# Optimization experiments

Measured on AMD Instinct MI355X. Metric: run time of the kernel, lower is better.

## Reference

```python
import jax, jax.numpy as jnp
import numpy as np

HIDDEN = 4096
NUM_Q = 32
NUM_KV = 8
HEAD_DIM = 128
EPS = 1e-6
ROPE_THETA = 1e6


def _rmsnorm(x, w):
    # x: [..., HEAD_DIM]
    var = jnp.mean(x * x, axis=-1, keepdims=True)
    return x * jax.lax.rsqrt(var + EPS) * w


def _rope(x, positions):
    # x: [n_tok, H, HEAD_DIM], rotate-half convention
    half = HEAD_DIM // 2
    inv_freq = 1.0 / (ROPE_THETA ** (jnp.arange(0, half, dtype=jnp.float32) / half))
    freqs = positions.astype(jnp.float32)[:, None] * inv_freq  # [n_tok, half]
    cos = jnp.concatenate([jnp.cos(freqs), jnp.cos(freqs)], axis=-1)[:, None, :]
    sin = jnp.concatenate([jnp.sin(freqs), jnp.sin(freqs)], axis=-1)[:, None, :]
    x1, x2 = x[..., :half], x[..., half:]
    rot = jnp.concatenate([-x2, x1], axis=-1)
    return x * cos + rot * sin


def setup_inputs() -> dict:
    key = jax.random.key(0)
    ks = jax.random.split(key, 7)
    n_tok = 2048
    s = 0.02
    return {
        "hidden": jax.random.normal(ks[0], (n_tok, HIDDEN), dtype=jnp.float32),
        "positions": jnp.arange(n_tok, dtype=jnp.int32),
        "Wq": jax.random.normal(ks[1], (HIDDEN, NUM_Q * HEAD_DIM), dtype=jnp.float32) * s,
        "Wk": jax.random.normal(ks[2], (HIDDEN, NUM_KV * HEAD_DIM), dtype=jnp.float32) * s,
        "Wv": jax.random.normal(ks[3], (HIDDEN, NUM_KV * HEAD_DIM), dtype=jnp.float32) * s,
        "Wo": jax.random.normal(ks[4], (NUM_Q * HEAD_DIM, HIDDEN), dtype=jnp.float32) * s,
        "q_norm_w": jnp.ones((HEAD_DIM,), dtype=jnp.float32),
        "k_norm_w": jnp.ones((HEAD_DIM,), dtype=jnp.float32),
    }


def reference(hidden, positions, Wq, Wk, Wv, Wo, q_norm_w, k_norm_w):
    n_tok = hidden.shape[0]
    group = NUM_Q // NUM_KV

    q = (hidden @ Wq).reshape(n_tok, NUM_Q, HEAD_DIM)
    k = (hidden @ Wk).reshape(n_tok, NUM_KV, HEAD_DIM)
    v = (hidden @ Wv).reshape(n_tok, NUM_KV, HEAD_DIM)

    q = _rmsnorm(q, q_norm_w)
    k = _rmsnorm(k, k_norm_w)
    q = _rope(q, positions)
    k = _rope(k, positions)

    # GQA: group q heads [n_tok, NUM_KV, group, HEAD_DIM]
    qg = q.reshape(n_tok, NUM_KV, group, HEAD_DIM)
    scale = 1.0 / np.sqrt(HEAD_DIM)
    scores = jnp.einsum("qhgd,khd->hgqk", qg, k) * scale  # [NUM_KV, group, n_tok, n_tok]
    causal = jnp.tril(jnp.ones((n_tok, n_tok), dtype=bool))
    scores = jnp.where(causal, scores, jnp.finfo(scores.dtype).min)
    probs = jax.nn.softmax(scores, axis=-1)
    out = jnp.einsum("hgqk,khd->qhgd", probs, v)  # [n_tok, NUM_KV, group, HEAD_DIM]
    out = out.reshape(n_tok, NUM_Q * HEAD_DIM)
    return out @ Wo
```

## Files before the change

kernel.cpp:

```cpp
#include <hip/hip_runtime.h>
#include <stdint.h>

typedef unsigned short u16;
typedef __bf16 bf16_t;
typedef bf16_t bf16x8 __attribute__((ext_vector_type(8)));
typedef float f32x4 __attribute__((ext_vector_type(4)));
typedef float f32x16 __attribute__((ext_vector_type(16)));
typedef u16 u16x4 __attribute__((ext_vector_type(4)));
typedef u16 u16x8 __attribute__((ext_vector_type(8)));
typedef uint32_t u32x4 __attribute__((ext_vector_type(4)));
typedef int i32x2 __attribute__((ext_vector_type(2)));

#define HIDDEN 4096
#define NTOK 2048
#define NQ 32
#define NKV 8
#define HD 128
#define QKV_N 6144

#define AS1 __attribute__((address_space(1)))
#define AS3 __attribute__((address_space(3)))

__device__ __forceinline__ u16 f2bf(float f) {
  union { float f; uint32_t u; } v; v.f = f;
  uint32_t u = v.u;
  return (u16)((u + 0x7fffu + ((u >> 16) & 1u)) >> 16);
}

__global__ void cvt_hidden(const float* __restrict__ src, u16* __restrict__ dst, int n4) {
  int i = blockIdx.x * blockDim.x + threadIdx.x;
  if (i >= n4) return;
  float4 v = ((const float4*)src)[i];
  u16x4 o;
  o[0] = f2bf(v.x); o[1] = f2bf(v.y); o[2] = f2bf(v.z); o[3] = f2bf(v.w);
  ((u16x4*)dst)[i] = o;
}

__global__ void transpose_cvt(const float* __restrict__ src, u16* __restrict__ dst,
                              int R, int C) {
  __shared__ float tile[64][65];
  int tx = threadIdx.x & 63;
  int ty = threadIdx.x >> 6;
  int r0 = blockIdx.y * 64, c0 = blockIdx.x * 64;
  for (int i = 0; i < 16; i++) {
    int r = ty + i * 4;
    tile[r][tx] = src[(size_t)(r0 + r) * C + c0 + tx];
  }
  __syncthreads();
  for (int i = 0; i < 16; i++) {
    int c = ty + i * 4;
    dst[(size_t)(c0 + c) * R + r0 + tx] = f2bf(tile[tx][c]);
  }
}

__global__ __launch_bounds__(256, 3) void gemm_bt(const u16* __restrict__ A,
                                                  const u16* __restrict__ B,
                                                  float* __restrict__ C,
                                                  int M, int N, int K) {
  __shared__ u16 sA[128 * 64];
  __shared__ u16 sB[128 * 64];
  const int tid = threadIdx.x;
  const int wave = tid >> 6, lane = tid & 63;
  const int quad = lane >> 4, l16 = lane & 15;
  const int wy = wave >> 1, wx = wave & 1;
  const int row0 = blockIdx.y * 128, col0 = blockIdx.x * 128;
  f32x4 acc[4][4] = {};
  const int lr = lane >> 3;
  const int sc = (lane & 7) ^ lr;
  const u16* gA = A + (size_t)(row0 + wave * 32 + lr) * K + sc * 8;
  const u16* gB = B + (size_t)(col0 + wave * 32 + lr) * K + sc * 8;
  u16* lA = sA + wave * 32 * 64;
  u16* lB = sB + wave * 32 * 64;
  const int swz = l16 & 7;
  for (int k0 = 0; k0 < K; k0 += 64) {
    for (int j = 0; j < 4; j++) {
      __builtin_amdgcn_global_load_lds(
          (AS1 void*)(void*)(gA + k0 + (size_t)(j * 8) * K),
          (AS3 void*)(void*)(lA + j * 8 * 64), 16, 0, 0);
      __builtin_amdgcn_global_load_lds(
          (AS1 void*)(void*)(gB + k0 + (size_t)(j * 8) * K),
          (AS3 void*)(void*)(lB + j * 8 * 64), 16, 0, 0);
    }
    __syncthreads();
    bf16x8 af[2][4], bfr[2][4];
    for (int s = 0; s < 2; s++)
      for (int mi = 0; mi < 4; mi++) {
        const int c = ((s * 4 + quad) ^ swz) * 8;
        af[s][mi] = *(const bf16x8*)(const void*)(sA + (wy * 64 + mi * 16 + l16) * 64 + c);
        bfr[s][mi] = *(const bf16x8*)(const void*)(sB + (wx * 64 + mi * 16 + l16) * 64 + c);
      }
    for (int s = 0; s < 2; s++)
      for (int mi = 0; mi < 4; mi++)
        for (int ni = 0; ni < 4; ni++)
          acc[mi][ni] = __builtin_amdgcn_mfma_f32_16x16x32_bf16(af[s][mi], bfr[s][ni], acc[mi][ni], 0, 0, 0);
    __syncthreads();
  }
  for (int mi = 0; mi < 4; mi++)
    for (int ni = 0; ni < 4; ni++) {
      int row = row0 + wy * 64 + mi * 16 + quad * 4;
      int col = col0 + wx * 64 + ni * 16 + l16;
      float* cp = C + (size_t)row * N + col;
      for (int r = 0; r < 4; r++) cp[(size_t)r * N] = acc[mi][ni][r];
    }
}

__global__ void normrope(const float* __restrict__ qkv, const int* __restrict__ pos,
                         const float* __restrict__ qw, const float* __restrict__ kw,
                         u16* __restrict__ Qo, u16* __restrict__ Ko) {
  const int hh = blockIdx.x;
  const int t = blockIdx.y * 4 + (threadIdx.x >> 6);
  const int lane = threadIdx.x & 63;
  const bool isQ = hh < NQ;
  const int col = isQ ? hh * HD : HIDDEN + (hh - NQ) * HD;
  const float* src = qkv + (size_t)t * QKV_N + col;
  float x1 = src[lane], x2 = src[lane + 64];
  float ss = x1 * x1 + x2 * x2;
  for (int m = 1; m < 64; m <<= 1) ss += __shfl_xor(ss, m);
  float inv = rsqrtf(ss * (1.0f / 128.0f) + 1e-6f);
  const float* w = isQ ? qw : kw;
  x1 *= inv * w[lane];
  x2 *= inv * w[lane + 64];
  float p = (float)pos[t];
  float freq = expf((float)lane * -0.2158673525f);
  float a = p * freq;
  float sn = sinf(a), cs = cosf(a);
  float o1 = x1 * cs - x2 * sn;
  float o2 = x2 * cs + x1 * sn;
  const float osc = isQ ? 0.08838834764831845f : 1.0f;
  u16* dst = isQ ? (Qo + (size_t)t * (NQ * HD) + hh * HD)
                 : (Ko + (size_t)t * (NKV * HD) + (hh - NQ) * HD);
  dst[lane] = f2bf(o1 * osc);
  dst[lane + 64] = f2bf(o2 * osc);
}

__global__ void vtrans(const float* __restrict__ qkv, u16* __restrict__ vT) {
  __shared__ float s[128][65];
  int tb = blockIdx.x;
  int vh = blockIdx.y;
  int tid = threadIdx.x;
  for (int i = 0; i < 32; i++) {
    int e = i * 256 + tid;
    int tl = e >> 7;
    int d = e & 127;
    s[d][tl] = qkv[(size_t)(tb * 64 + tl) * QKV_N + 5120 + vh * 128 + d];
  }
  __syncthreads();
  for (int i = 0; i < 32; i++) {
    int e = i * 256 + tid;
    int d = e >> 6;
    int tl = e & 63;
    vT[(size_t)vh * (HD * NTOK) + (size_t)d * NTOK + tb * 64 + tl] = f2bf(s[d][tl]);
  }
}

__global__ __launch_bounds__(512, 2) void flash3(const u16* __restrict__ Q,
                                                 const u16* __restrict__ K,
                                                 const u16* __restrict__ V,
                                                 u16* __restrict__ O) {
  __shared__ u16 sK[64 * 136];
  __shared__ u16 sV[128 * 72];
  const int lid = blockIdx.x;
  const int kvh = lid & 7;
  const int head = kvh * 4 + ((lid >> 3) & 3);
  const int p = lid >> 5;
  const int tid = threadIdx.x;
  const int wave = tid >> 6, lane = tid & 63;
  const int l32 = lane & 31, h = lane >> 5;
  const int tileq = (wave < 4) ? p : (15 - p);
  const int qrow0 = tileq * 128 + (wave & 3) * 32;
  const u16* Vh = V + (size_t)kvh * (HD * NTOK);

  bf16x8 qf[8];
  const u16* qbase = Q + (size_t)(qrow0 + l32) * (NQ * HD) + head * HD + h * 8;
#pragma unroll
  for (int ks = 0; ks < 8; ks++)
    qf[ks] = *(const bf16x8*)(const void*)(qbase + ks * 16);

  f32x16 accO[4] = {};
  float l_loc = 0.f;
  const int nU = 32 - 2 * p;
  const int rk0 = tid >> 4, ck0 = tid & 15;
  const int rv0 = tid >> 3, cv0 = tid & 7;
  const u16* Kr = K + (size_t)kvh * HD + ck0 * 8;
  const u16* Vr = Vh + (size_t)rv0 * NTOK + cv0 * 8;
  const u16* Vr2 = Vh + (size_t)(rv0 + 64) * NTOK + cv0 * 8;

  u16x8 k0 = *(const u16x8*)(const void*)(Kr + (size_t)rk0 * (NKV * HD));
  u16x8 k1 = *(const u16x8*)(const void*)(Kr + (size_t)(rk0 + 32) * (NKV * HD));
  u16x8 v0 = *(const u16x8*)(const void*)(Vr);
  u16x8 v1 = *(const u16x8*)(const void*)(Vr2);

  for (int kb = 0; kb < nU; kb++) {
    __syncthreads();
    *(u16x8*)(void*)(sK + rk0 * 136 + ck0 * 8) = k0;
    *(u16x8*)(void*)(sK + (rk0 + 32) * 136 + ck0 * 8) = k1;
    *(u16x8*)(void*)(sV + rv0 * 72 + cv0 * 8) = v0;
    *(u16x8*)(void*)(sV + (rv0 + 64) * 72 + cv0 * 8) = v1;
    __syncthreads();
    if (kb + 1 < nU) {
      const size_t koff = (size_t)((kb + 1) * 64) * (NKV * HD);
      k0 = *(const u16x8*)(const void*)(Kr + koff + (size_t)rk0 * (NKV * HD));
      k1 = *(const u16x8*)(const void*)(Kr + koff + (size_t)(rk0 + 32) * (NKV * HD));
      v0 = *(const u16x8*)(const void*)(Vr + (kb + 1) * 64);
      v1 = *(const u16x8*)(const void*)(Vr2 + (kb + 1) * 64);
    }
    const int t0 = kb * 64;
    if (t0 > qrow0 + 31) continue;
    const bool act1 = (t0 + 32 <= qrow0 + 31);

    f32x16 s0 = {}, s1 = {};
#pragma unroll
    for (int ks = 0; ks < 8; ks++) {
      bf16x8 kf0 = *(const bf16x8*)(const void*)(sK + l32 * 136 + ks * 16 + h * 8);
      s0 = __builtin_amdgcn_mfma_f32_32x32x16_bf16(kf0, qf[ks], s0, 0, 0, 0);
    }
    if (act1) {
#pragma unroll
      for (int ks = 0; ks < 8; ks++) {
        bf16x8 kf1 = *(const bf16x8*)(const void*)(sK + (32 + l32) * 136 + ks * 16 + h * 8);
        s1 = __builtin_amdgcn_mfma_f32_32x32x16_bf16(kf1, qf[ks], s1, 0, 0, 0);
      }
    }

    auto process = [&](const f32x16& sv_, int tb) {
      float pr[16];
      const int tbase = t0 + tb * 32;
      const int qg = qrow0 + l32;
      if (tbase + 31 <= qrow0) {
#pragma unroll
        for (int r = 0; r < 16; r++) { float e = __expf(sv_[r]); pr[r] = e; l_loc += e; }
      } else {
#pragma unroll
        for (int r = 0; r < 16; r++) {
          const int tok = tbase + (r & 3) + 8 * (r >> 2) + 4 * h;
          float e = (tok <= qg) ? __expf(sv_[r]) : 0.f;
          pr[r] = e; l_loc += e;
        }
      }
#pragma unroll
      for (int u = 0; u < 2; u++) {
        uint32_t A0, A1, B0, B1;
        asm("v_cvt_pk_bf16_f32 %0, %1, %2" : "=v"(A0) : "v"(pr[u * 8 + 0]), "v"(pr[u * 8 + 1]));
        asm("v_cvt_pk_bf16_f32 %0, %1, %2" : "=v"(A1) : "v"(pr[u * 8 + 2]), "v"(pr[u * 8 + 3]));
        asm("v_cvt_pk_bf16_f32 %0, %1, %2" : "=v"(B0) : "v"(pr[u * 8 + 4]), "v"(pr[u * 8 + 5]));
        asm("v_cvt_pk_bf16_f32 %0, %1, %2" : "=v"(B1) : "v"(pr[u * 8 + 6]), "v"(pr[u * 8 + 7]));
#if __has_builtin(__builtin_amdgcn_permlane32_swap)
        i32x2 r02 = __builtin_amdgcn_permlane32_swap((int)A0, (int)B0, false, false);
        i32x2 r13 = __builtin_amdgcn_permlane32_swap((int)A1, (int)B1, false, false);
        const uint32_t w0 = (uint32_t)r02.x, w2 = (uint32_t)r02.y;
        const uint32_t w1 = (uint32_t)r13.x, w3 = (uint32_t)r13.y;
#else
        const uint32_t A0x = (uint32_t)__shfl_xor((int)A0, 32);
        const uint32_t A1x = (uint32_t)__shfl_xor((int)A1, 32);
        const uint32_t B0x = (uint32_t)__shfl_xor((int)B0, 32);
        const uint32_t B1x = (uint32_t)__shfl_xor((int)B1, 32);
        const uint32_t w0 = h ? B0x : A0;
        const uint32_t w1 = h ? B1x : A1;
        const uint32_t w2 = h ? B0 : A0x;
        const uint32_t w3 = h ? B1 : A1x;
#endif
        union { u32x4 w; bf16x8 v; } pf;
        pf.w = (u32x4){w0, w1, w2, w3};
#pragma unroll
        for (int db = 0; db < 4; db++) {
          bf16x8 vf = *(const bf16x8*)(const void*)(sV + (db * 32 + l32) * 72 + tb * 32 + u * 16 + h * 8);
          accO[db] = __builtin_amdgcn_mfma_f32_32x32x16_bf16(vf, pf.v, accO[db], 0, 0, 0);
        }
      }
    };
    process(s0, 0);
    if (act1) process(s1, 1);
  }

  l_loc += __shfl_xor(l_loc, 32);
  const float inv = 1.0f / l_loc;
  u16* ob = O + (size_t)(qrow0 + l32) * (NQ * HD) + head * HD;
#pragma unroll
  for (int db = 0; db < 4; db++)
#pragma unroll
    for (int g = 0; g < 4; g++) {
      u16x4 o4;
#pragma unroll
      for (int j = 0; j < 4; j++) o4[j] = f2bf(accO[db][4 * g + j] * inv);
      *(u16x4*)(void*)(ob + db * 32 + g * 8 + h * 4) = o4;
    }
}

extern "C" void kernel_launch(void* const* d_in, const int* in_sizes, int n_in,
                              void* d_out, int out_size, void* d_ws, size_t ws_size,
                              hipStream_t stream) {
  const float* hidden = (const float*)d_in[0];
  const int* positions = (const int*)d_in[1];
  const float* Wq = (const float*)d_in[2];
  const float* Wk = (const float*)d_in[3];
  const float* Wv = (const float*)d_in[4];
  const float* Wo = (const float*)d_in[5];
  const float* qw = (const float*)d_in[6];
  const float* kw = (const float*)d_in[7];
  char* ws = (char*)d_ws;
  u16* hid_bf  = (u16*)(ws);
  u16* WqkvT   = (u16*)(ws + 16777216);
  u16* WoT     = (u16*)(ws + 67108864);
  float* qkvf  = (float*)(ws + 100663296);
  u16* Qn      = (u16*)(ws + 150994944);
  u16* Kn      = (u16*)(ws + 167772160);
  u16* Vt      = (u16*)(ws + 171966464);
  u16* AO      = (u16*)(ws + 176160768);
  float* outp  = (float*)d_out;

  cvt_hidden<<<NTOK * HIDDEN / 4 / 256, 256, 0, stream>>>(hidden, hid_bf, NTOK * HIDDEN / 4);
  transpose_cvt<<<dim3(64, 64), 256, 0, stream>>>(Wq, WqkvT, 4096, 4096);
  transpose_cvt<<<dim3(16, 64), 256, 0, stream>>>(Wk, WqkvT + (size_t)4096 * 4096, 4096, 1024);
  transpose_cvt<<<dim3(16, 64), 256, 0, stream>>>(Wv, WqkvT + (size_t)5120 * 4096, 4096, 1024);
  transpose_cvt<<<dim3(64, 64), 256, 0, stream>>>(Wo, WoT, 4096, 4096);
  gemm_bt<<<dim3(48, 16), 256, 0, stream>>>(hid_bf, WqkvT, qkvf, 2048, 6144, 4096);
  normrope<<<dim3(40, 512), 256, 0, stream>>>(qkvf, positions, qw, kw, Qn, Kn);
  vtrans<<<dim3(32, 8), 256, 0, stream>>>(qkvf, Vt);
  flash3<<<dim3(256), 512, 0, stream>>>(Qn, Kn, Vt, AO);
  gemm_bt<<<dim3(32, 16), 256, 0, stream>>>(AO, WoT, outp, 2048, 4096, 4096);
}
```

Measured before the change: 479.3 us.

## Replace 128x128 GEMM with double-buffered 256x256 tile pipelined GEMM

Replaces the simple single-buffered 128x128 bf16 GEMM with a 256x256-tile, 512-thread kernel. It double-buffers LDS and interleaves global-to-LDS staging of the next K-tile with MFMA on quarter-tiles, using explicit barriers, waitcnts and setprio. The goal is to hide load latency and raise arithmetic intensity for both the QKV and output projections. The trade-off is heavier LDS use (128KB) and fewer blocks: 192 and 128 blocks on 256 CUs, so some CUs sit idle.

```diff
diff --git a/kernel.cpp b/kernel.cpp
--- a/kernel.cpp
+++ b/kernel.cpp
@@ -53,53 +53,108 @@
   }
 }
 
-__global__ __launch_bounds__(256, 3) void gemm_bt(const u16* __restrict__ A,
+#define BARRIER() do { asm volatile("" ::: "memory"); __builtin_amdgcn_s_barrier(); asm volatile("" ::: "memory"); } while (0)
+#define WAIT_LGKM0() asm volatile("s_waitcnt lgkmcnt(0)" ::: "memory")
+#define WAIT_VM4() asm volatile("s_waitcnt vmcnt(4)" ::: "memory")
+#define WAIT_VM0() asm volatile("s_waitcnt vmcnt(0)" ::: "memory")
+
+#define STAGE_A(buf, half, t) do { \
+  __builtin_amdgcn_global_load_lds((AS1 void*)(void*)(gA + (size_t)((half) * 128) * K + (t) * 64), \
+      (AS3 void*)(void*)(&sA[buf][((half) * 128) * 64 + lds0]), 16, 0, 0); \
+  __builtin_amdgcn_global_load_lds((AS1 void*)(void*)(gA + (size_t)((half) * 128 + 64) * K + (t) * 64), \
+      (AS3 void*)(void*)(&sA[buf][((half) * 128 + 64) * 64 + lds0]), 16, 0, 0); \
+} while (0)
+
+#define STAGE_B(buf, half, t) do { \
+  __builtin_amdgcn_global_load_lds((AS1 void*)(void*)(gB + (size_t)((half) * 128) * K + (t) * 64), \
+      (AS3 void*)(void*)(&sB[buf][((half) * 128) * 64 + lds0]), 16, 0, 0); \
+  __builtin_amdgcn_global_load_lds((AS1 void*)(void*)(gB + (size_t)((half) * 128 + 64) * K + (t) * 64), \
+      (AS3 void*)(void*)(&sB[buf][((half) * 128 + 64) * 64 + lds0]), 16, 0, 0); \
+} while (0)
+
+#define RD_A(buf, mh, dst) do { \
+  _Pragma("unroll") for (int m_ = 0; m_ < 4; m_++) \
+  _Pragma("unroll") for (int s_ = 0; s_ < 2; s_++) \
+    dst[m_][s_] = *(const bf16x8*)(const void*)(&sA[buf][(wy * 128 + ((mh) * 4 + m_) * 16 + l16) * 64 + ((s_ * 4 + quad) ^ swz) * 8]); \
+} while (0)
+
+#define RD_B(buf, nh, dst) do { \
+  _Pragma("unroll") for (int n_ = 0; n_ < 2; n_++) \
+  _Pragma("unroll") for (int s_ = 0; s_ < 2; s_++) \
+    dst[n_][s_] = *(const bf16x8*)(const void*)(&sB[buf][(wx * 64 + ((nh) * 2 + n_) * 16 + l16) * 64 + ((s_ * 4 + quad) ^ swz) * 8]); \
+} while (0)
+
+#define MFMA16(mh, nh, a_, b_) do { \
+  __builtin_amdgcn_s_setprio(1); \
+  _Pragma("unroll") for (int s_ = 0; s_ < 2; s_++) \
+  _Pragma("unroll") for (int m_ = 0; m_ < 4; m_++) \
+  _Pragma("unroll") for (int n_ = 0; n_ < 2; n_++) \
+    acc[(mh) * 4 + m_][(nh) * 2 + n_] = __builtin_amdgcn_mfma_f32_16x16x32_bf16( \
+        a_[m_][s_], b_[n_][s_], acc[(mh) * 4 + m_][(nh) * 2 + n_], 0, 0, 0); \
+  __builtin_amdgcn_s_setprio(0); \
+} while (0)
+
+__global__ __launch_bounds__(512, 2) void gemm256(const u16* __restrict__ A,
                                                   const u16* __restrict__ B,
                                                   float* __restrict__ C,
                                                   int M, int N, int K) {
-  __shared__ u16 sA[128 * 64];
-  __shared__ u16 sB[128 * 64];
+  __shared__ u16 sA[2][256 * 64];
+  __shared__ u16 sB[2][256 * 64];
   const int tid = threadIdx.x;
   const int wave = tid >> 6, lane = tid & 63;
   const int quad = lane >> 4, l16 = lane & 15;
-  const int wy = wave >> 1, wx = wave & 1;
-  const int row0 = blockIdx.y * 128, col0 = blockIdx.x * 128;
-  f32x4 acc[4][4] = {};
-  const int lr = lane >> 3;
-  const int sc = (lane & 7) ^ lr;
-  const u16* gA = A + (size_t)(row0 + wave * 32 + lr) * K + sc * 8;
-  const u16* gB = B + (size_t)(col0 + wave * 32 + lr) * K + sc * 8;
-  u16* lA = sA + wave * 32 * 64;
-  u16* lB = sB + wave * 32 * 64;
+  const int wy = wave >> 2, wx = wave & 3;
+  const int row0 = blockIdx.y * 256, col0 = blockIdx.x * 256;
+  f32x4 acc[8][4] = {};
+  const int srow = tid >> 3, schunk = tid & 7;
+  const int gchunk = schunk ^ (srow & 7);
+  const u16* gA = A + (size_t)(row0 + srow) * K + gchunk * 8;
+  const u16* gB = B + (size_t)(col0 + srow) * K + gchunk * 8;
+  const int lds0 = srow * 64 + schunk * 8;
   const int swz = l16 & 7;
-  for (int k0 = 0; k0 < K; k0 += 64) {
-    for (int j = 0; j < 4; j++) {
-      __builtin_amdgcn_global_load_lds(
-          (AS1 void*)(void*)(gA + k0 + (size_t)(j * 8) * K),
-          (AS3 void*)(void*)(lA + j * 8 * 64), 16, 0, 0);
-      __builtin_amdgcn_global_load_lds(
-          (AS1 void*)(void*)(gB + k0 + (size_t)(j * 8) * K),
-          (AS3 void*)(void*)(lB + j * 8 * 64), 16, 0, 0);
-    }
-    __syncthreads();
-    bf16x8 af[2][4], bfr[2][4];
-    for (int s = 0; s < 2; s++)
-      for (int mi = 0; mi < 4; mi++) {
-        const int c = ((s * 4 + quad) ^ swz) * 8;
-        af[s][mi] = *(const bf16x8*)(const void*)(sA + (wy * 64 + mi * 16 + l16) * 64 + c);
-        bfr[s][mi] = *(const bf16x8*)(const void*)(sB + (wx * 64 + mi * 16 + l16) * 64 + c);
-      }
-    for (int s = 0; s < 2; s++)
-      for (int mi = 0; mi < 4; mi++)
-        for (int ni = 0; ni < 4; ni++)
-          acc[mi][ni] = __builtin_amdgcn_mfma_f32_16x16x32_bf16(af[s][mi], bfr[s][ni], acc[mi][ni], 0, 0, 0);
-    __syncthreads();
-  }
-  for (int mi = 0; mi < 4; mi++)
+
+  STAGE_B(0, 0, 0); STAGE_B(0, 1, 0); STAGE_A(0, 0, 0); STAGE_A(0, 1, 0);
+  STAGE_B(1, 0, 1); STAGE_B(1, 1, 1);
+  WAIT_VM4();
+  BARRIER();
+
+  const int nIter = (K >> 6) >> 1;
+  for (int i = 0; i < nIter; i++) {
+    const int tb = 2 * i + 1, t2 = 2 * i + 2, t3 = 2 * i + 3;
+    const bool more = (i + 1 < nIter);
+    bf16x8 a0[4][2], a1[4][2], b0[2][2], b1[2][2];
+    RD_A(0, 0, a0); RD_B(0, 0, b0);
+    STAGE_A(1, 0, tb);
+    BARRIER(); WAIT_LGKM0(); MFMA16(0, 0, a0, b0); BARRIER();
+    RD_B(0, 1, b1);
+    STAGE_A(1, 1, tb);
+    BARRIER(); WAIT_LGKM0(); MFMA16(0, 1, a0, b1); BARRIER();
+    RD_A(0, 1, a1);
+    if (more) STAGE_B(0, 0, t2);
+    BARRIER(); WAIT_LGKM0(); MFMA16(1, 1, a1, b1); BARRIER();
+    if (more) { STAGE_B(0, 1, t2); WAIT_VM4(); } else { WAIT_VM0(); }
+    BARRIER(); MFMA16(1, 0, a1, b0); BARRIER();
+    RD_A(1, 0, a0); RD_B(1, 0, b0);
+    if (more) STAGE_A(0, 0, t2);
+    BARRIER(); WAIT_LGKM0(); MFMA16(0, 0, a0, b0); BARRIER();
+    RD_B(1, 1, b1);
+    if (more) STAGE_A(0, 1, t2);
+    BARRIER(); WAIT_LGKM0(); MFMA16(0, 1, a0, b1); BARRIER();
+    RD_A(1, 1, a1);
+    if (more) STAGE_B(1, 0, t3);
+    BARRIER(); WAIT_LGKM0(); MFMA16(1, 1, a1, b1); BARRIER();
+    if (more) { STAGE_B(1, 1, t3); WAIT_VM4(); }
+    BARRIER(); MFMA16(1, 0, a1, b0); BARRIER();
+  }
+
+#pragma unroll
+  for (int mi = 0; mi < 8; mi++)
+#pragma unroll
     for (int ni = 0; ni < 4; ni++) {
-      int row = row0 + wy * 64 + mi * 16 + quad * 4;
+      int row = row0 + wy * 128 + mi * 16 + quad * 4;
       int col = col0 + wx * 64 + ni * 16 + l16;
       float* cp = C + (size_t)row * N + col;
+#pragma unroll
       for (int r = 0; r < 4; r++) cp[(size_t)r * N] = acc[mi][ni][r];
     }
 }
@@ -313,9 +368,9 @@
   transpose_cvt<<<dim3(16, 64), 256, 0, stream>>>(Wk, WqkvT + (size_t)4096 * 4096, 4096, 1024);
   transpose_cvt<<<dim3(16, 64), 256, 0, stream>>>(Wv, WqkvT + (size_t)5120 * 4096, 4096, 1024);
   transpose_cvt<<<dim3(64, 64), 256, 0, stream>>>(Wo, WoT, 4096, 4096);
-  gemm_bt<<<dim3(48, 16), 256, 0, stream>>>(hid_bf, WqkvT, qkvf, 2048, 6144, 4096);
+  gemm256<<<dim3(24, 8), 512, 0, stream>>>(hid_bf, WqkvT, qkvf, 2048, 6144, 4096);
   normrope<<<dim3(40, 512), 256, 0, stream>>>(qkvf, positions, qw, kw, Qn, Kn);
   vtrans<<<dim3(32, 8), 256, 0, stream>>>(qkvf, Vt);
   flash3<<<dim3(256), 512, 0, stream>>>(Qn, Kn, Vt, AO);
-  gemm_bt<<<dim3(32, 16), 256, 0, stream>>>(AO, WoT, outp, 2048, 4096, 4096);
-}
+  gemm256<<<dim3(16, 8), 512, 0, stream>>>(AO, WoT, outp, 2048, 4096, 4096);
+}
```

Result: slower. 551.8 us (+15.1%).
